# Performance work log

Hardware: AMD Instinct MI355X
Metric: run time of the kernel (lower is better)

## Reference

```python
import jax, jax.numpy as jnp
import numpy as np

K_BITS = 128  # hash bits (k in __init__)
WORD = 32     # pack bits into uint32 words -> K_BITS // WORD = 4 words


def _pack_bits(bits_u32):
    # bits_u32: [N, K_BITS] uint32 in {0,1} -> [N, K_BITS//WORD] uint32 keys
    N = bits_u32.shape[0]
    b = bits_u32.reshape(N, K_BITS // WORD, WORD)
    shifts = jnp.arange(WORD, dtype=jnp.uint32)
    return jnp.sum(jnp.left_shift(b, shifts), axis=-1, dtype=jnp.uint32)  # [N, 4]


def setup_inputs() -> dict:
    key = jax.random.key(0)
    k1, k2 = jax.random.split(key)
    T, B, D = 128, 64, 4096
    latent_state = jax.random.normal(k1, (T, B, D), dtype=jnp.float32)
    A = jax.random.normal(k2, (K_BITS, D), dtype=jnp.float32)  # fixed random projection buffer
    return {"latent_state": latent_state, "A": A}


def reference(latent_state, A):
    # latent_state: [T, B, D]; A: [k, D]. Returns intrinsic reward [T, B].
    T, B, D = latent_state.shape
    flat = latent_state.reshape(T * B, D)                    # detach is a no-op for fwd
    proj = flat @ A.T                                        # [N, k]
    bits = (proj > 0).astype(jnp.uint32)                     # SimHash sign bits
    words = _pack_bits(bits)                                 # [N, 4] collision-free 128-bit key

    # counts dict starts empty each run: visit count of row i is the number of
    # rows j <= i with an identical key (keys processed in row order).
    N = words.shape[0]
    eq = jnp.ones((N, N), dtype=bool)
    for w in range(K_BITS // WORD):  # small fixed loop over 4 key words
        eq = eq & (words[:, None, w] == words[None, :, w])
    counts = jnp.tril(eq).sum(axis=1)                        # [N] int, >= 1
    intrinsic = 1.0 / jnp.sqrt(counts.astype(latent_state.dtype))
    return intrinsic.reshape(T, B)
```

## Files before the change

kernel.cpp:

```cpp
#include <hip/hip_runtime.h>
#include <stdint.h>

#define D_DIM 4096
#define N_ROWS 8192

typedef __attribute__((ext_vector_type(8))) short bfrag8;
typedef __attribute__((ext_vector_type(4))) float facc4;
typedef unsigned long long u64;

__device__ __forceinline__ uint32_t pack_bf16x2(float lo, float hi) {
    union { float f; uint32_t u; } a, b;
    a.f = lo; b.f = hi;
    return (b.u & 0xFFFF0000u) | (a.u >> 16);
}

__global__ void __launch_bounds__(256)
prep_A(const float* __restrict__ A, uint32_t* __restrict__ A_sw) {
    const int S = blockIdx.x * 256 + threadIdx.x;
    const int c = S >> 10;
    const int s = S & 1023;
    const int n = s >> 3;
    const int g = (s & 7) ^ (n & 7);
    const float* src = A + (size_t)n * D_DIM + c * 64 + g * 8;
    float4 f0 = *(const float4*)(src);
    float4 f1 = *(const float4*)(src + 4);
    uint4 o;
    o.x = pack_bf16x2(f0.x, f0.y);
    o.y = pack_bf16x2(f0.z, f0.w);
    o.z = pack_bf16x2(f1.x, f1.y);
    o.w = pack_bf16x2(f1.z, f1.w);
    *(uint4*)(A_sw + (size_t)S * 4) = o;
}

__global__ void __launch_bounds__(256, 2)
gemm_split128(const float* __restrict__ L, const uint32_t* __restrict__ A_sw,
              float* __restrict__ partials, int kpb) {
    __shared__ ushort Ls[128 * 72];
    __shared__ uint4  As[1024];

    const int tid  = threadIdx.x;
    const int wave = tid >> 6;
    const int lane = tid & 63;
    const int split = blockIdx.x;
    const int row0 = blockIdx.y * 128;
    const int c  = lane & 15;
    const int q  = lane >> 4;
    const int wm = wave >> 1;
    const int wn = wave & 1;

    const int lrow = tid >> 3;
    const int lf4  = tid & 7;
    const float* lsrc = L + (size_t)(row0 + lrow) * D_DIM + lf4 * 4;
    ushort* ldst = &Ls[lrow * 72 + lf4 * 4];

    facc4 acc[4][4];
#pragma unroll
    for (int m = 0; m < 4; m++)
#pragma unroll
        for (int ct = 0; ct < 4; ct++) acc[m][ct] = (facc4){0.f, 0.f, 0.f, 0.f};

    const int kc0 = split * kpb * 64;
    const int kc1 = kc0 + kpb * 64;
    for (int kc = kc0; kc < kc1; kc += 64) {
        const uint32_t* gA = A_sw + (size_t)(kc >> 6) * 4096;
#pragma unroll
        for (int i = 0; i < 4; i++) {
            const int slot0 = wave * 256 + i * 64;
            __builtin_amdgcn_global_load_lds(
                (const __attribute__((address_space(1))) uint32_t*)(gA + (slot0 + lane) * 4),
                (__attribute__((address_space(3))) uint32_t*)(&As[slot0]),
                16, 0, 0);
        }
#pragma unroll
        for (int i = 0; i < 4; i++) {
            const float* p = lsrc + (size_t)i * 32 * D_DIM + kc;
            float4 f0 = *(const float4*)(p);
            float4 f1 = *(const float4*)(p + 32);
            *(uint2*)(ldst + i * 32 * 72) =
                make_uint2(pack_bf16x2(f0.x, f0.y), pack_bf16x2(f0.z, f0.w));
            *(uint2*)(ldst + i * 32 * 72 + 32) =
                make_uint2(pack_bf16x2(f1.x, f1.y), pack_bf16x2(f1.z, f1.w));
        }
        __syncthreads();

#pragma unroll
        for (int ks = 0; ks < 2; ks++) {
            bfrag8 a[4];
#pragma unroll
            for (int m = 0; m < 4; m++)
                a[m] = *(const bfrag8*)&Ls[(64 * wm + 16 * m + c) * 72 + ks * 32 + q * 8];
#pragma unroll
            for (int ct = 0; ct < 4; ct++) {
                const int n  = 64 * wn + 16 * ct + c;
                const int gl = ks * 4 + q;
                bfrag8 b = *(const bfrag8*)&As[n * 8 + (gl ^ (n & 7))];
#pragma unroll
                for (int m = 0; m < 4; m++)
                    acc[m][ct] = __builtin_amdgcn_mfma_f32_16x16x32_bf16(a[m], b, acc[m][ct], 0, 0, 0);
            }
        }
        __syncthreads();
    }

    float* P = partials + ((size_t)split * N_ROWS * 128);
    const int cb = 64 * wn + c;
#pragma unroll
    for (int m = 0; m < 4; m++) {
        const int rb = row0 + 64 * wm + 16 * m + 4 * q;
#pragma unroll
        for (int ct = 0; ct < 4; ct++)
#pragma unroll
            for (int r = 0; r < 4; r++)
                P[(size_t)(rb + r) * 128 + cb + 16 * ct] = acc[m][ct][r];
    }
}

__global__ void __launch_bounds__(256)
reduce_pack(const float* __restrict__ partials, u64* __restrict__ folded, int S) {
    const int row  = blockIdx.x * 4 + (threadIdx.x >> 6);
    const int lane = threadIdx.x & 63;
    float s0 = 0.f, s1 = 0.f;
    for (int s = 0; s < S; s++) {
        const float* P = partials + ((size_t)s * N_ROWS * 128) + (size_t)row * 128;
        s0 += P[lane];
        s1 += P[lane + 64];
    }
    u64 b0 = __ballot(s0 > 0.0f);
    u64 b1 = __ballot(s1 > 0.0f);
    if (lane == 0) folded[row] = b0 ^ b1;
}

__global__ void __launch_bounds__(512)
count_rows(const u64* __restrict__ folded, float* __restrict__ out) {
    __shared__ u64 K[N_ROWS];
    const int tid = threadIdx.x;
    for (int i = tid; i < N_ROWS; i += 512) K[i] = folded[i];
    __syncthreads();

    const int g    = blockIdx.x * 8 + (tid >> 6);
    const int lane = tid & 63;
    int rows[4];
    u64 my[4];
    int cnt[4] = {0, 0, 0, 0};
#pragma unroll
    for (int r = 0; r < 4; r++) {
        rows[r] = g + 2048 * r;
        my[r] = K[rows[r]];
    }
    const int maxrow = rows[3];
    for (int j = lane; j <= maxrow; j += 64) {
        u64 k = K[j];
#pragma unroll
        for (int r = 0; r < 4; r++)
            cnt[r] += (int)((j <= rows[r]) & (k == my[r]));
    }
#pragma unroll
    for (int r = 0; r < 4; r++) {
        int v = cnt[r];
#pragma unroll
        for (int o = 32; o; o >>= 1) v += __shfl_xor(v, o, 64);
        if (lane == 0) out[rows[r]] = rsqrtf((float)v);
    }
}

extern "C" void kernel_launch(void* const* d_in, const int* in_sizes, int n_in,
                              void* d_out, int out_size, void* d_ws, size_t ws_size,
                              hipStream_t stream) {
    const float* latent = (const float*)d_in[0];
    const float* A      = (const float*)d_in[1];
    float* out          = (float*)d_out;

    uint32_t* A_sw = (uint32_t*)d_ws;
    u64* folded = (u64*)((char*)d_ws + (1 << 20));
    float* partials = (float*)((char*)d_ws + (1 << 20) + (1 << 16));

    const size_t base = (1 << 20) + (1 << 16);
    const size_t per_split = (size_t)N_ROWS * 128 * sizeof(float);
    int S = 1;
    if (ws_size >= base + 8 * per_split)      S = 8;
    else if (ws_size >= base + 4 * per_split) S = 4;
    else if (ws_size >= base + 2 * per_split) S = 2;

    prep_A<<<256, 256, 0, stream>>>(A, A_sw);
    gemm_split128<<<dim3(S, 64), 256, 0, stream>>>(latent, A_sw, partials, 64 / S);
    reduce_pack<<<2048, 256, 0, stream>>>(partials, folded, S);
    count_rows<<<256, 512, 0, stream>>>(folded, out);
}
```

Measured before the change: 234.3 us.

## Replace LDS-tiled GEMM with single-wave 16-row tiles reading B from global

The 128x128 block-tiled GEMM, which staged L and A through shared memory with barriers, is replaced by a one-wave-per-block kernel. Each wave computes a 16-row by 128-column tile, loading its L fragment directly into registers and its pre-swizzled A fragments directly from global/L2. This removes LDS staging and __syncthreads and raises the block count to 512 x S. The cost is that every wave re-reads the full A slice from cache, so B traffic grows roughly eightfold, and each loaded B fragment feeds only one MFMA.

```diff
diff --git a/kernel.cpp b/kernel.cpp
--- a/kernel.cpp
+++ b/kernel.cpp
@@ -7,6 +7,8 @@
 typedef __attribute__((ext_vector_type(8))) short bfrag8;
 typedef __attribute__((ext_vector_type(4))) float facc4;
 typedef unsigned long long u64;
+
+union ABfrag { uint32_t u[4]; bfrag8 b; };
 
 __device__ __forceinline__ uint32_t pack_bf16x2(float lo, float hi) {
     union { float f; uint32_t u; } a, b;
@@ -32,87 +34,62 @@
     *(uint4*)(A_sw + (size_t)S * 4) = o;
 }
 
-__global__ void __launch_bounds__(256, 2)
-gemm_split128(const float* __restrict__ L, const uint32_t* __restrict__ A_sw,
-              float* __restrict__ partials, int kpb) {
-    __shared__ ushort Ls[128 * 72];
-    __shared__ uint4  As[1024];
+__global__ void __launch_bounds__(64, 4)
+gemm_wave(const float* __restrict__ L, const uint32_t* __restrict__ A_sw,
+          float* __restrict__ partials, int nchunk) {
+    const int lane  = threadIdx.x;
+    const int split = blockIdx.x;
+    const int row0  = blockIdx.y * 16;
+    const int c = lane & 15;
+    const int q = lane >> 4;
 
-    const int tid  = threadIdx.x;
-    const int wave = tid >> 6;
-    const int lane = tid & 63;
-    const int split = blockIdx.x;
-    const int row0 = blockIdx.y * 128;
-    const int c  = lane & 15;
-    const int q  = lane >> 4;
-    const int wm = wave >> 1;
-    const int wn = wave & 1;
+    const int kc0 = split * nchunk;
+    const float* Lrow = L + (size_t)(row0 + c) * D_DIM + (size_t)kc0 * 64 + q * 8;
+    const uint32_t* gB0 = A_sw + (size_t)kc0 * 4096 + c * 32;
+    const int sw0 = (q ^ (c & 7)) * 4;
+    const int sw1 = ((4 + q) ^ (c & 7)) * 4;
 
-    const int lrow = tid >> 3;
-    const int lf4  = tid & 7;
-    const float* lsrc = L + (size_t)(row0 + lrow) * D_DIM + lf4 * 4;
-    ushort* ldst = &Ls[lrow * 72 + lf4 * 4];
+    facc4 acc[8];
+#pragma unroll
+    for (int i = 0; i < 8; i++) acc[i] = (facc4){0.f, 0.f, 0.f, 0.f};
 
-    facc4 acc[4][4];
+#pragma unroll 2
+    for (int t = 0; t < nchunk; t++) {
+        const float* p = Lrow + t * 64;
+        float4 f0 = *(const float4*)(p);
+        float4 f1 = *(const float4*)(p + 4);
+        float4 f2 = *(const float4*)(p + 32);
+        float4 f3 = *(const float4*)(p + 36);
+
+        ABfrag a0, a1;
+        a0.u[0] = pack_bf16x2(f0.x, f0.y);
+        a0.u[1] = pack_bf16x2(f0.z, f0.w);
+        a0.u[2] = pack_bf16x2(f1.x, f1.y);
+        a0.u[3] = pack_bf16x2(f1.z, f1.w);
+        a1.u[0] = pack_bf16x2(f2.x, f2.y);
+        a1.u[1] = pack_bf16x2(f2.z, f2.w);
+        a1.u[2] = pack_bf16x2(f3.x, f3.y);
+        a1.u[3] = pack_bf16x2(f3.z, f3.w);
+
+        const uint32_t* gB = gB0 + (size_t)t * 4096;
 #pragma unroll
-    for (int m = 0; m < 4; m++)
-#pragma unroll
-        for (int ct = 0; ct < 4; ct++) acc[m][ct] = (facc4){0.f, 0.f, 0.f, 0.f};
-
-    const int kc0 = split * kpb * 64;
-    const int kc1 = kc0 + kpb * 64;
-    for (int kc = kc0; kc < kc1; kc += 64) {
-        const uint32_t* gA = A_sw + (size_t)(kc >> 6) * 4096;
-#pragma unroll
-        for (int i = 0; i < 4; i++) {
-            const int slot0 = wave * 256 + i * 64;
-            __builtin_amdgcn_global_load_lds(
-                (const __attribute__((address_space(1))) uint32_t*)(gA + (slot0 + lane) * 4),
-                (__attribute__((address_space(3))) uint32_t*)(&As[slot0]),
-                16, 0, 0);
+        for (int ct = 0; ct < 8; ct++) {
+            bfrag8 b0 = *(const bfrag8*)(gB + ct * 512 + sw0);
+            acc[ct] = __builtin_amdgcn_mfma_f32_16x16x32_bf16(a0.b, b0, acc[ct], 0, 0, 0);
         }
 #pragma unroll
-        for (int i = 0; i < 4; i++) {
-            const float* p = lsrc + (size_t)i * 32 * D_DIM + kc;
-            float4 f0 = *(const float4*)(p);
-            float4 f1 = *(const float4*)(p + 32);
-            *(uint2*)(ldst + i * 32 * 72) =
-                make_uint2(pack_bf16x2(f0.x, f0.y), pack_bf16x2(f0.z, f0.w));
-            *(uint2*)(ldst + i * 32 * 72 + 32) =
-                make_uint2(pack_bf16x2(f1.x, f1.y), pack_bf16x2(f1.z, f1.w));
+        for (int ct = 0; ct < 8; ct++) {
+            bfrag8 b1 = *(const bfrag8*)(gB + ct * 512 + sw1);
+            acc[ct] = __builtin_amdgcn_mfma_f32_16x16x32_bf16(a1.b, b1, acc[ct], 0, 0, 0);
         }
-        __syncthreads();
-
-#pragma unroll
-        for (int ks = 0; ks < 2; ks++) {
-            bfrag8 a[4];
-#pragma unroll
-            for (int m = 0; m < 4; m++)
-                a[m] = *(const bfrag8*)&Ls[(64 * wm + 16 * m + c) * 72 + ks * 32 + q * 8];
-#pragma unroll
-            for (int ct = 0; ct < 4; ct++) {
-                const int n  = 64 * wn + 16 * ct + c;
-                const int gl = ks * 4 + q;
-                bfrag8 b = *(const bfrag8*)&As[n * 8 + (gl ^ (n & 7))];
-#pragma unroll
-                for (int m = 0; m < 4; m++)
-                    acc[m][ct] = __builtin_amdgcn_mfma_f32_16x16x32_bf16(a[m], b, acc[m][ct], 0, 0, 0);
-            }
-        }
-        __syncthreads();
     }
 
-    float* P = partials + ((size_t)split * N_ROWS * 128);
-    const int cb = 64 * wn + c;
+    float* P = partials + (size_t)split * N_ROWS * 128 + (size_t)row0 * 128;
 #pragma unroll
-    for (int m = 0; m < 4; m++) {
-        const int rb = row0 + 64 * wm + 16 * m + 4 * q;
+    for (int ct = 0; ct < 8; ct++)
 #pragma unroll
-        for (int ct = 0; ct < 4; ct++)
-#pragma unroll
-            for (int r = 0; r < 4; r++)
-                P[(size_t)(rb + r) * 128 + cb + 16 * ct] = acc[m][ct][r];
-    }
+        for (int r = 0; r < 4; r++)
+            P[(size_t)(4 * q + r) * 128 + 16 * ct + c] = acc[ct][r];
 }
 
 __global__ void __launch_bounds__(256)
@@ -182,7 +159,7 @@
     else if (ws_size >= base + 2 * per_split) S = 2;
 
     prep_A<<<256, 256, 0, stream>>>(A, A_sw);
-    gemm_split128<<<dim3(S, 64), 256, 0, stream>>>(latent, A_sw, partials, 64 / S);
+    gemm_wave<<<dim3(S, 512), 64, 0, stream>>>(latent, A_sw, partials, 64 / S);
     reduce_pack<<<2048, 256, 0, stream>>>(partials, folded, S);
     count_rows<<<256, 512, 0, stream>>>(folded, out);
 }
```

New measurement: 245.8 us. 1.05x slower.

## Load latent tiles directly to LDS as fp32 and convert to bf16 at fragment read

Applied to the files above, without the earlier changes.

The latent tile is now copied from global memory straight into shared memory in fp32 with global_load_lds, using an XOR-swizzled layout. Previously each tile went through registers for bf16 packing before being stored. The bf16 conversion now happens when MFMA A-fragments are read from LDS. This removes the register round trip and lets the latent loads run asynchronously like the A loads, at the cost of doubling LDS usage for the L tile and repeating the pack work per wave.

```diff
diff --git a/kernel.cpp b/kernel.cpp
--- a/kernel.cpp
+++ b/kernel.cpp
@@ -7,6 +7,8 @@
 typedef __attribute__((ext_vector_type(8))) short bfrag8;
 typedef __attribute__((ext_vector_type(4))) float facc4;
 typedef unsigned long long u64;
+
+union ABfrag { uint32_t u[4]; bfrag8 b; };
 
 __device__ __forceinline__ uint32_t pack_bf16x2(float lo, float hi) {
     union { float f; uint32_t u; } a, b;
@@ -35,8 +37,8 @@
 __global__ void __launch_bounds__(256, 2)
 gemm_split128(const float* __restrict__ L, const uint32_t* __restrict__ A_sw,
               float* __restrict__ partials, int kpb) {
-    __shared__ ushort Ls[128 * 72];
-    __shared__ uint4  As[1024];
+    __shared__ uint32_t Lf[8192];
+    __shared__ uint4    As[1024];
 
     const int tid  = threadIdx.x;
     const int wave = tid >> 6;
@@ -48,10 +50,9 @@
     const int wm = wave >> 1;
     const int wn = wave & 1;
 
-    const int lrow = tid >> 3;
-    const int lf4  = tid & 7;
-    const float* lsrc = L + (size_t)(row0 + lrow) * D_DIM + lf4 * 4;
-    ushort* ldst = &Ls[lrow * 72 + lf4 * 4];
+    const int lrow_lo = wave * 4 + (lane >> 4);
+    const int js      = (lane & 15) ^ (lrow_lo & 7);
+    const float* lsrc0 = L + (size_t)(row0 + lrow_lo) * D_DIM + js * 4;
 
     facc4 acc[4][4];
 #pragma unroll
@@ -72,23 +73,29 @@
                 16, 0, 0);
         }
 #pragma unroll
-        for (int i = 0; i < 4; i++) {
-            const float* p = lsrc + (size_t)i * 32 * D_DIM + kc;
-            float4 f0 = *(const float4*)(p);
-            float4 f1 = *(const float4*)(p + 32);
-            *(uint2*)(ldst + i * 32 * 72) =
-                make_uint2(pack_bf16x2(f0.x, f0.y), pack_bf16x2(f0.z, f0.w));
-            *(uint2*)(ldst + i * 32 * 72 + 32) =
-                make_uint2(pack_bf16x2(f1.x, f1.y), pack_bf16x2(f1.z, f1.w));
+        for (int i = 0; i < 8; i++) {
+            const uint32_t* src = (const uint32_t*)(lsrc0 + (size_t)(i * 16) * D_DIM + kc);
+            __builtin_amdgcn_global_load_lds(
+                (const __attribute__((address_space(1))) uint32_t*)src,
+                (__attribute__((address_space(3))) uint32_t*)(&Lf[(i * 256 + wave * 64) * 4]),
+                16, 0, 0);
         }
         __syncthreads();
 
 #pragma unroll
         for (int ks = 0; ks < 2; ks++) {
-            bfrag8 a[4];
+            ABfrag a[4];
 #pragma unroll
-            for (int m = 0; m < 4; m++)
-                a[m] = *(const bfrag8*)&Ls[(64 * wm + 16 * m + c) * 72 + ks * 32 + q * 8];
+            for (int m = 0; m < 4; m++) {
+                const int rr = 64 * wm + 16 * m + c;
+                const int j0 = ks * 8 + q * 2;
+                const float4 f0 = *(const float4*)&Lf[rr * 64 + ((j0    ) ^ (c & 7)) * 4];
+                const float4 f1 = *(const float4*)&Lf[rr * 64 + ((j0 + 1) ^ (c & 7)) * 4];
+                a[m].u[0] = pack_bf16x2(f0.x, f0.y);
+                a[m].u[1] = pack_bf16x2(f0.z, f0.w);
+                a[m].u[2] = pack_bf16x2(f1.x, f1.y);
+                a[m].u[3] = pack_bf16x2(f1.z, f1.w);
+            }
 #pragma unroll
             for (int ct = 0; ct < 4; ct++) {
                 const int n  = 64 * wn + 16 * ct + c;
@@ -96,7 +103,7 @@
                 bfrag8 b = *(const bfrag8*)&As[n * 8 + (gl ^ (n & 7))];
 #pragma unroll
                 for (int m = 0; m < 4; m++)
-                    acc[m][ct] = __builtin_amdgcn_mfma_f32_16x16x32_bf16(a[m], b, acc[m][ct], 0, 0, 0);
+                    acc[m][ct] = __builtin_amdgcn_mfma_f32_16x16x32_bf16(a[m].b, b, acc[m][ct], 0, 0, 0);
             }
         }
         __syncthreads();
```

Result: faster. 223.8 us (-4.5%).
